# Kernel tuning notes

Measured on AMD Instinct MI355X. Metric: run time of the kernel, lower is better.

Reference implementation:

```python
import jax, jax.numpy as jnp
import numpy as np

WS = 8          # window_size
HEADS = 8
HEAD_DIM = 32
DIM = 256
INNER = HEADS * HEAD_DIM  # 256
STRIDE = 2 * WS - 1       # 15


def _rel_idx_1d():
    # coords of the WS*WS pixels in a window
    coords = np.array([[x, y] for x in range(WS) for y in range(WS)], dtype=np.int32)
    rel = coords[None, :, :] - coords[:, None, :] + (WS - 1)   # [WS^2, WS^2, 2] in [0, 2WS-2]
    idx = rel[:, :, 0] * STRIDE + rel[:, :, 1]
    return jnp.asarray(np.clip(idx, 0, None).reshape(-1), dtype=jnp.int32)

_REL_IDX = _rel_idx_1d()  # [WS^2 * WS^2]


def setup_inputs() -> dict:
    key = jax.random.key(0)
    ks = jax.random.split(key, 5)
    b, l, H, W = 2, 4, 128, 128
    x = jax.random.normal(ks[0], (b, l, H, W, DIM), dtype=jnp.float32)
    W_qkv = jax.random.normal(ks[1], (DIM, 3 * INNER), dtype=jnp.float32) * (DIM ** -0.5)
    W_out = jax.random.normal(ks[2], (INNER, DIM), dtype=jnp.float32) * (INNER ** -0.5)
    b_out = jax.random.normal(ks[3], (DIM,), dtype=jnp.float32) * 0.02
    pos_emb = jax.random.normal(ks[4], (STRIDE, STRIDE), dtype=jnp.float32)
    return {"x": x, "W_qkv": W_qkv, "W_out": W_out, "b_out": b_out, "pos_emb": pos_emb}


def _to_windows(t, b, l, nh, nw):
    # [b,l,H,W,INNER] -> [b,l,heads,nh*nw,WS*WS,head_dim]
    t = t.reshape(b, l, nh, WS, nw, WS, HEADS, HEAD_DIM)
    t = t.transpose(0, 1, 6, 2, 4, 3, 5, 7)  # b l h nh nw ws ws d
    return t.reshape(b, l, HEADS, nh * nw, WS * WS, HEAD_DIM)


def reference(x, W_qkv, W_out, b_out, pos_emb):
    b, l, H, W, _ = x.shape
    nh, nw = H // WS, W // WS
    scale = HEAD_DIM ** -0.5

    qkv = x @ W_qkv                               # [b,l,H,W,3*INNER]
    q, k, v = jnp.split(qkv, 3, axis=-1)
    q = _to_windows(q, b, l, nh, nw)
    k = _to_windows(k, b, l, nh, nw)
    v = _to_windows(v, b, l, nh, nw)

    # per-window attention scores: [b,l,heads,windows,WS^2,WS^2]
    dots = jnp.einsum('blhwid,blhwjd->blhwij', q, k) * scale
    bias = pos_emb.reshape(-1)[_REL_IDX].reshape(WS * WS, WS * WS)
    dots = dots + bias

    attn = jax.nn.softmax(dots, axis=-1)
    out = jnp.einsum('blhwij,blhwjd->blhwid', attn, v)  # [b,l,heads,windows,WS^2,hd]

    # back to [b,l,H,W,INNER]
    out = out.reshape(b, l, HEADS, nh, nw, WS, WS, HEAD_DIM)
    out = out.transpose(0, 1, 3, 5, 4, 6, 2, 7)  # b l nh ws nw ws h d
    out = out.reshape(b, l, nh * WS, nw * WS, INNER)

    return out @ W_out + b_out  # dropout is identity at eval
```

## Files before the change

### kernel.cpp

```cpp
#include <hip/hip_runtime.h>
#include <hip/hip_bf16.h>

typedef short bf16x8 __attribute__((ext_vector_type(8)));
typedef float f32x4  __attribute__((ext_vector_type(4)));
typedef unsigned short u16;
typedef unsigned int u32;

#define MFMA16(a, b, c) __builtin_amdgcn_mfma_f32_16x16x32_bf16((a), (b), (c), 0, 0, 0)

static __device__ __forceinline__ u16 f2b(float f) {
  __hip_bfloat16 h = __float2bfloat16(f);
  return __builtin_bit_cast(u16, h);
}
static __device__ __forceinline__ float b2f(u16 v) {
  unsigned int u = ((unsigned int)v) << 16;
  return __builtin_bit_cast(float, u);
}
static __device__ __forceinline__ u32 pk2(float a, float b) {
  return (u32)f2b(a) | ((u32)f2b(b) << 16);
}

union FragU { uint4 u; bf16x8 v; };

static __device__ __forceinline__ bf16x8 shufx(uint2 lo, uint2 hi,
                                               int sA4, int sB4, bool uh) {
  u32 l0 = (u32)__builtin_amdgcn_ds_bpermute(sA4, (int)lo.x);
  u32 l1 = (u32)__builtin_amdgcn_ds_bpermute(sA4, (int)lo.y);
  u32 h0 = (u32)__builtin_amdgcn_ds_bpermute(sA4, (int)hi.x);
  u32 h1 = (u32)__builtin_amdgcn_ds_bpermute(sA4, (int)hi.y);
  u32 l2 = (u32)__builtin_amdgcn_ds_bpermute(sB4, (int)lo.x);
  u32 l3 = (u32)__builtin_amdgcn_ds_bpermute(sB4, (int)lo.y);
  u32 h2 = (u32)__builtin_amdgcn_ds_bpermute(sB4, (int)hi.x);
  u32 h3 = (u32)__builtin_amdgcn_ds_bpermute(sB4, (int)hi.y);
  FragU f;
  f.u.x = uh ? h0 : l0;  f.u.y = uh ? h1 : l1;
  f.u.z = uh ? h2 : l2;  f.u.w = uh ? h3 : l3;
  return f.v;
}

__global__ void prep(const float* __restrict__ wqkv, const float* __restrict__ wout,
                     const float* __restrict__ pos, u16* __restrict__ wqkT,
                     u16* __restrict__ wvB, u16* __restrict__ woutB,
                     u16* __restrict__ biasQ) {
  const int b = blockIdx.x, t = threadIdx.x;
  const float s = 0.17677669529663689f;
  if (b < 128) {
    int e0 = b * 1024 + t * 4;
#pragma unroll
    for (int i = 0; i < 4; ++i) {
      int e = e0 + i, o = e >> 8, ii = e & 255;
      float v = wqkv[(size_t)ii * 768 + o];
      wqkT[e] = f2b(o < 256 ? v * s : v);
    }
  } else if (b < 192) {
    int e0 = (b - 128) * 1024 + t * 4;
#pragma unroll
    for (int i = 0; i < 4; ++i) {
      int e = e0 + i, frag = e >> 9, w = e & 511, lane = w >> 3, ee = w & 7;
      int k8 = frag >> 4, np = frag & 15;
      int k = k8 * 32 + ((lane >> 4) << 3) + ee;
      int col = 512 + np * 16 + (lane & 15);
      wvB[e] = f2b(wqkv[(size_t)k * 768 + col]);
    }
  } else if (b < 256) {
    int e0 = (b - 192) * 1024 + t * 4;
#pragma unroll
    for (int i = 0; i < 4; ++i) {
      int e = e0 + i, frag = e >> 9, w = e & 511, lane = w >> 3, ee = w & 7;
      int k8 = frag >> 4, np = frag & 15;
      int k = k8 * 32 + ((lane >> 4) << 3) + ee;
      int col = np * 16 + (lane & 15);
      woutB[e] = f2b(wout[(size_t)k * 256 + col]);
    }
  } else {
    int e0 = (b - 256) * 1024 + t * 4;
#pragma unroll
    for (int i = 0; i < 4; ++i) {
      int e = e0 + i, iq = e >> 6, jk = e & 63;
      int ix = iq >> 3, iy = iq & 7, jx = jk >> 3, jy = jk & 7;
      biasQ[e] = f2b(pos[(jx - ix + 7) * 15 + (jy - iy + 7)]);
    }
  }
}

__global__ __launch_bounds__(512, 4)
void winattn(const float* __restrict__ x,
             const u16* __restrict__ wqkT,
             const u16* __restrict__ wvB,
             const u16* __restrict__ woutB,
             const float* __restrict__ b_out,
             const u16* __restrict__ biasQ,
             float* __restrict__ out) {
  __shared__ u16 Xs[64][264];
  __shared__ u16 VTs[256][72];
  __shared__ u16 Bs[64][68];

  const int tid  = threadIdx.x;
  const int lane = tid & 63;
  const int h    = tid >> 6;
  const int c    = lane & 15;
  const int g    = lane >> 4;

  const int win = blockIdx.x;
  const int img = win >> 8;
  const int wid = win & 255;
  const int py0 = (wid >> 4) << 3;
  const int px0 = (wid & 15) << 3;
  const size_t imgbase = (size_t)img * (128 * 128);

  const f32x4 fz = {0.f, 0.f, 0.f, 0.f};

#pragma unroll
  for (int it = 0; it < 8; ++it) {
    int ch = tid + it * 512;
    int row = ch >> 6, c4 = (ch & 63) << 2;
    int py = py0 + (row >> 3), px = px0 + (row & 7);
    const float4 v = *reinterpret_cast<const float4*>(
        x + ((size_t)(imgbase + py * 128 + px)) * 256 + c4);
    ushort4 pk{f2b(v.x), f2b(v.y), f2b(v.z), f2b(v.w)};
    *reinterpret_cast<ushort4*>(&Xs[row][c4]) = pk;
  }
  {
    int row = tid >> 3, c0 = (tid & 7) * 8;
    *reinterpret_cast<ushort4*>(&Bs[row][c0]) =
        *reinterpret_cast<const ushort4*>(biasQ + row * 64 + c0);
    *reinterpret_cast<ushort4*>(&Bs[row][c0 + 4]) =
        *reinterpret_cast<const ushort4*>(biasQ + row * 64 + c0 + 4);
  }
  __syncthreads();

  const int sA4 = (c + 16 * ((2 * g) & 3)) * 4;
  const int sB4 = (c + 16 * ((2 * g + 1) & 3)) * 4;
  const bool uh = g >= 2;

  const int hq = h * 32, hk = 256 + h * 32;

  bf16x8 qf[4];
  {
    f32x4 aq[2][4];
#pragma unroll
    for (int mt = 0; mt < 2; ++mt)
#pragma unroll
      for (int nt = 0; nt < 4; ++nt) aq[mt][nt] = fz;
#pragma unroll 2
    for (int k8 = 0; k8 < 8; ++k8) {
      bf16x8 xb[4];
#pragma unroll
      for (int nt = 0; nt < 4; ++nt)
        xb[nt] = *reinterpret_cast<const bf16x8*>(&Xs[nt * 16 + c][k8 * 32 + g * 8]);
      bf16x8 wq[2];
#pragma unroll
      for (int mt = 0; mt < 2; ++mt)
        wq[mt] = *reinterpret_cast<const bf16x8*>(
            wqkT + (size_t)(hq + mt * 16 + c) * 256 + k8 * 32 + g * 8);
#pragma unroll
      for (int mt = 0; mt < 2; ++mt)
#pragma unroll
        for (int nt = 0; nt < 4; ++nt)
          aq[mt][nt] = MFMA16(wq[mt], xb[nt], aq[mt][nt]);
    }
#pragma unroll
    for (int t4 = 0; t4 < 4; ++t4) {
      uint2 lo{pk2(aq[0][t4][0], aq[0][t4][1]), pk2(aq[0][t4][2], aq[0][t4][3])};
      uint2 hi{pk2(aq[1][t4][0], aq[1][t4][1]), pk2(aq[1][t4][2], aq[1][t4][3])};
      qf[t4] = shufx(lo, hi, sA4, sB4, uh);
    }
  }

  bf16x8 kf[4];
  {
    f32x4 ak[2][4];
#pragma unroll
    for (int mt = 0; mt < 2; ++mt)
#pragma unroll
      for (int nt = 0; nt < 4; ++nt) ak[mt][nt] = fz;
#pragma unroll 2
    for (int k8 = 0; k8 < 8; ++k8) {
      bf16x8 xb[4];
#pragma unroll
      for (int nt = 0; nt < 4; ++nt)
        xb[nt] = *reinterpret_cast<const bf16x8*>(&Xs[nt * 16 + c][k8 * 32 + g * 8]);
      bf16x8 wk[2];
#pragma unroll
      for (int mt = 0; mt < 2; ++mt)
        wk[mt] = *reinterpret_cast<const bf16x8*>(
            wqkT + (size_t)(hk + mt * 16 + c) * 256 + k8 * 32 + g * 8);
#pragma unroll
      for (int mt = 0; mt < 2; ++mt)
#pragma unroll
        for (int nt = 0; nt < 4; ++nt)
          ak[mt][nt] = MFMA16(wk[mt], xb[nt], ak[mt][nt]);
    }
#pragma unroll
    for (int t4 = 0; t4 < 4; ++t4) {
      uint2 lo{pk2(ak[0][t4][0], ak[0][t4][1]), pk2(ak[0][t4][2], ak[0][t4][3])};
      uint2 hi{pk2(ak[1][t4][0], ak[1][t4][1]), pk2(ak[1][t4][2], ak[1][t4][3])};
      kf[t4] = shufx(lo, hi, sA4, sB4, uh);
    }
  }

  {
    f32x4 av[4][2];
#pragma unroll
    for (int mt = 0; mt < 4; ++mt)
#pragma unroll
      for (int j = 0; j < 2; ++j) av[mt][j] = fz;
#pragma unroll 1
    for (int k8 = 0; k8 < 8; ++k8) {
      bf16x8 xb[4];
#pragma unroll
      for (int mt = 0; mt < 4; ++mt)
        xb[mt] = *reinterpret_cast<const bf16x8*>(&Xs[mt * 16 + c][k8 * 32 + g * 8]);
      bf16x8 bv[2];
#pragma unroll
      for (int j = 0; j < 2; ++j)
        bv[j] = *reinterpret_cast<const bf16x8*>(
            wvB + (size_t)((k8 * 16 + 2 * h + j) * 64 + lane) * 8);
#pragma unroll
      for (int mt = 0; mt < 4; ++mt)
#pragma unroll
        for (int j = 0; j < 2; ++j)
          av[mt][j] = MFMA16(xb[mt], bv[j], av[mt][j]);
    }
#pragma unroll
    for (int j = 0; j < 2; ++j)
#pragma unroll
      for (int mt = 0; mt < 4; ++mt) {
        ushort4 pk{f2b(av[mt][j][0]), f2b(av[mt][j][1]),
                   f2b(av[mt][j][2]), f2b(av[mt][j][3])};
        *reinterpret_cast<ushort4*>(&VTs[(2 * h + j) * 16 + c][mt * 16 + 4 * g]) = pk;
      }
  }

  bf16x8 vf[2][2];
#pragma unroll
  for (int kk = 0; kk < 2; ++kk)
#pragma unroll
    for (int dt = 0; dt < 2; ++dt)
      vf[kk][dt] = *reinterpret_cast<const bf16x8*>(
          &VTs[h * 32 + dt * 16 + c][kk * 32 + g * 8]);

  __builtin_amdgcn_s_setprio(1);
  ushort4 ao[8];
#pragma unroll
  for (int tqt = 0; tqt < 4; ++tqt) {
    f32x4 stq[4];
#pragma unroll
    for (int tkt = 0; tkt < 4; ++tkt) {
      const ushort4 bb = *reinterpret_cast<const ushort4*>(
          &Bs[tqt * 16 + c][tkt * 16 + 4 * g]);
      const f32x4 bf = {b2f(bb.x), b2f(bb.y), b2f(bb.z), b2f(bb.w)};
      stq[tkt] = MFMA16(kf[tkt], qf[tqt], bf);
    }
    float m0 = fmaxf(fmaxf(stq[0][0], stq[0][1]), fmaxf(stq[0][2], stq[0][3]));
    float m1 = fmaxf(fmaxf(stq[1][0], stq[1][1]), fmaxf(stq[1][2], stq[1][3]));
    float m2 = fmaxf(fmaxf(stq[2][0], stq[2][1]), fmaxf(stq[2][2], stq[2][3]));
    float m3 = fmaxf(fmaxf(stq[3][0], stq[3][1]), fmaxf(stq[3][2], stq[3][3]));
    float mx = fmaxf(fmaxf(m0, m1), fmaxf(m2, m3));
    mx = fmaxf(mx, __shfl_xor(mx, 16));
    mx = fmaxf(mx, __shfl_xor(mx, 32));
#pragma unroll
    for (int tkt = 0; tkt < 4; ++tkt)
#pragma unroll
      for (int r = 0; r < 4; ++r)
        stq[tkt][r] = __expf(stq[tkt][r] - mx);
    float s0 = (stq[0][0] + stq[0][1]) + (stq[0][2] + stq[0][3]);
    float s1 = (stq[1][0] + stq[1][1]) + (stq[1][2] + stq[1][3]);
    float s2 = (stq[2][0] + stq[2][1]) + (stq[2][2] + stq[2][3]);
    float s3 = (stq[3][0] + stq[3][1]) + (stq[3][2] + stq[3][3]);
    float sum = (s0 + s1) + (s2 + s3);
    sum += __shfl_xor(sum, 16);
    sum += __shfl_xor(sum, 32);
    const float rs = 1.0f / sum;

    f32x4 o0 = fz, o1 = fz;
#pragma unroll
    for (int kk = 0; kk < 2; ++kk) {
      uint2 lo{pk2(stq[2 * kk][0], stq[2 * kk][1]),
               pk2(stq[2 * kk][2], stq[2 * kk][3])};
      uint2 hi{pk2(stq[2 * kk + 1][0], stq[2 * kk + 1][1]),
               pk2(stq[2 * kk + 1][2], stq[2 * kk + 1][3])};
      bf16x8 pf = shufx(lo, hi, sA4, sB4, uh);
      o0 = MFMA16(vf[kk][0], pf, o0);
      o1 = MFMA16(vf[kk][1], pf, o1);
    }
    ao[tqt]     = ushort4{f2b(o0[0] * rs), f2b(o0[1] * rs),
                          f2b(o0[2] * rs), f2b(o0[3] * rs)};
    ao[4 + tqt] = ushort4{f2b(o1[0] * rs), f2b(o1[1] * rs),
                          f2b(o1[2] * rs), f2b(o1[3] * rs)};
  }
  __builtin_amdgcn_s_setprio(0);

  __syncthreads();
#pragma unroll
  for (int dt = 0; dt < 2; ++dt)
#pragma unroll
    for (int tqt = 0; tqt < 4; ++tqt)
      *reinterpret_cast<ushort4*>(&Xs[c + 16 * tqt][h * 32 + 16 * dt + 4 * g]) =
          ao[dt * 4 + tqt];
  __syncthreads();

  f32x4 yc[4][2];
#pragma unroll
  for (int mt = 0; mt < 4; ++mt)
#pragma unroll
    for (int jj = 0; jj < 2; ++jj) yc[mt][jj] = fz;
#pragma unroll 2
  for (int k8 = 0; k8 < 8; ++k8) {
    bf16x8 af[4];
#pragma unroll
    for (int mt = 0; mt < 4; ++mt)
      af[mt] = *reinterpret_cast<const bf16x8*>(&Xs[mt * 16 + c][k8 * 32 + g * 8]);
    bf16x8 bw[2];
#pragma unroll
    for (int jj = 0; jj < 2; ++jj) {
      int nt = h * 2 + jj;
      bw[jj] = *reinterpret_cast<const bf16x8*>(
          woutB + (size_t)((k8 * 16 + nt) * 64 + lane) * 8);
    }
#pragma unroll
    for (int mt = 0; mt < 4; ++mt)
#pragma unroll
      for (int jj = 0; jj < 2; ++jj)
        yc[mt][jj] = MFMA16(af[mt], bw[jj], yc[mt][jj]);
  }
#pragma unroll
  for (int jj = 0; jj < 2; ++jj) {
    const int nt = h * 2 + jj;
    const float bo = b_out[nt * 16 + c];
#pragma unroll
    for (int mt = 0; mt < 4; ++mt)
#pragma unroll
      for (int r = 0; r < 4; ++r) {
        int row = mt * 16 + g * 4 + r;
        int py = py0 + (row >> 3), px = px0 + (row & 7);
        out[((size_t)(imgbase + py * 128 + px)) * 256 + nt * 16 + c] =
            yc[mt][jj][r] + bo;
      }
  }
}

extern "C" void kernel_launch(void* const* d_in, const int* in_sizes, int n_in,
                              void* d_out, int out_size, void* d_ws, size_t ws_size,
                              hipStream_t stream) {
  const float* x    = (const float*)d_in[0];
  const float* wqkv = (const float*)d_in[1];
  const float* wout = (const float*)d_in[2];
  const float* bout = (const float*)d_in[3];
  const float* pos  = (const float*)d_in[4];
  float* out = (float*)d_out;

  u16* wqkT  = (u16*)d_ws;
  u16* wvB   = wqkT + 512 * 256;
  u16* woutB = wvB + 65536;
  u16* biasQ = woutB + 65536;

  prep<<<260, 256, 0, stream>>>(wqkv, wout, pos, wqkT, wvB, woutB, biasQ);
  winattn<<<2048, 512, 0, stream>>>(x, wqkT, wvB, woutB, bout, biasQ, out);
}
```

Before: 138.9 us.

## Drop VTs shared buffer, build V fragments in registers, raise occupancy

V projection output is now shuffled straight into MFMA B-fragments in registers instead of going through a transposed shared-memory buffer. This removes about 36KB of LDS per block. Q and K projections are computed one half at a time to cut live accumulators, and attention outputs are written directly into Xs after a barrier. Launch bounds request 6 blocks per CU. The combined aim is higher occupancy, at the risk of register spills or a worse MFMA schedule from the smaller per-iteration tiles.

```diff
diff --git a/kernel.cpp b/kernel.cpp
--- a/kernel.cpp
+++ b/kernel.cpp
@@ -83,7 +83,7 @@
   }
 }
 
-__global__ __launch_bounds__(512, 4)
+__global__ __launch_bounds__(512, 6)
 void winattn(const float* __restrict__ x,
              const u16* __restrict__ wqkT,
              const u16* __restrict__ wvB,
@@ -92,7 +92,6 @@
              const u16* __restrict__ biasQ,
              float* __restrict__ out) {
   __shared__ u16 Xs[64][264];
-  __shared__ u16 VTs[256][72];
   __shared__ u16 Bs[64][68];
 
   const int tid  = threadIdx.x;
@@ -135,70 +134,7 @@
 
   const int hq = h * 32, hk = 256 + h * 32;
 
-  bf16x8 qf[4];
-  {
-    f32x4 aq[2][4];
-#pragma unroll
-    for (int mt = 0; mt < 2; ++mt)
-#pragma unroll
-      for (int nt = 0; nt < 4; ++nt) aq[mt][nt] = fz;
-#pragma unroll 2
-    for (int k8 = 0; k8 < 8; ++k8) {
-      bf16x8 xb[4];
-#pragma unroll
-      for (int nt = 0; nt < 4; ++nt)
-        xb[nt] = *reinterpret_cast<const bf16x8*>(&Xs[nt * 16 + c][k8 * 32 + g * 8]);
-      bf16x8 wq[2];
-#pragma unroll
-      for (int mt = 0; mt < 2; ++mt)
-        wq[mt] = *reinterpret_cast<const bf16x8*>(
-            wqkT + (size_t)(hq + mt * 16 + c) * 256 + k8 * 32 + g * 8);
-#pragma unroll
-      for (int mt = 0; mt < 2; ++mt)
-#pragma unroll
-        for (int nt = 0; nt < 4; ++nt)
-          aq[mt][nt] = MFMA16(wq[mt], xb[nt], aq[mt][nt]);
-    }
-#pragma unroll
-    for (int t4 = 0; t4 < 4; ++t4) {
-      uint2 lo{pk2(aq[0][t4][0], aq[0][t4][1]), pk2(aq[0][t4][2], aq[0][t4][3])};
-      uint2 hi{pk2(aq[1][t4][0], aq[1][t4][1]), pk2(aq[1][t4][2], aq[1][t4][3])};
-      qf[t4] = shufx(lo, hi, sA4, sB4, uh);
-    }
-  }
-
-  bf16x8 kf[4];
-  {
-    f32x4 ak[2][4];
-#pragma unroll
-    for (int mt = 0; mt < 2; ++mt)
-#pragma unroll
-      for (int nt = 0; nt < 4; ++nt) ak[mt][nt] = fz;
-#pragma unroll 2
-    for (int k8 = 0; k8 < 8; ++k8) {
-      bf16x8 xb[4];
-#pragma unroll
-      for (int nt = 0; nt < 4; ++nt)
-        xb[nt] = *reinterpret_cast<const bf16x8*>(&Xs[nt * 16 + c][k8 * 32 + g * 8]);
-      bf16x8 wk[2];
-#pragma unroll
-      for (int mt = 0; mt < 2; ++mt)
-        wk[mt] = *reinterpret_cast<const bf16x8*>(
-            wqkT + (size_t)(hk + mt * 16 + c) * 256 + k8 * 32 + g * 8);
-#pragma unroll
-      for (int mt = 0; mt < 2; ++mt)
-#pragma unroll
-        for (int nt = 0; nt < 4; ++nt)
-          ak[mt][nt] = MFMA16(wk[mt], xb[nt], ak[mt][nt]);
-    }
-#pragma unroll
-    for (int t4 = 0; t4 < 4; ++t4) {
-      uint2 lo{pk2(ak[0][t4][0], ak[0][t4][1]), pk2(ak[0][t4][2], ak[0][t4][3])};
-      uint2 hi{pk2(ak[1][t4][0], ak[1][t4][1]), pk2(ak[1][t4][2], ak[1][t4][3])};
-      kf[t4] = shufx(lo, hi, sA4, sB4, uh);
-    }
-  }
-
+  bf16x8 vf[2][2];
   {
     f32x4 av[4][2];
 #pragma unroll
@@ -225,23 +161,80 @@
 #pragma unroll
     for (int j = 0; j < 2; ++j)
 #pragma unroll
-      for (int mt = 0; mt < 4; ++mt) {
-        ushort4 pk{f2b(av[mt][j][0]), f2b(av[mt][j][1]),
-                   f2b(av[mt][j][2]), f2b(av[mt][j][3])};
-        *reinterpret_cast<ushort4*>(&VTs[(2 * h + j) * 16 + c][mt * 16 + 4 * g]) = pk;
-      }
-  }
-
-  bf16x8 vf[2][2];
-#pragma unroll
-  for (int kk = 0; kk < 2; ++kk)
-#pragma unroll
-    for (int dt = 0; dt < 2; ++dt)
-      vf[kk][dt] = *reinterpret_cast<const bf16x8*>(
-          &VTs[h * 32 + dt * 16 + c][kk * 32 + g * 8]);
+      for (int kk = 0; kk < 2; ++kk) {
+        uint2 lo{pk2(av[2 * kk][j][0], av[2 * kk][j][1]),
+                 pk2(av[2 * kk][j][2], av[2 * kk][j][3])};
+        uint2 hi{pk2(av[2 * kk + 1][j][0], av[2 * kk + 1][j][1]),
+                 pk2(av[2 * kk + 1][j][2], av[2 * kk + 1][j][3])};
+        vf[kk][j] = shufx(lo, hi, sA4, sB4, uh);
+      }
+  }
+
+  bf16x8 qf[4];
+  {
+    uint2 qlo[4], qhi[4];
+#pragma unroll
+    for (int mt = 0; mt < 2; ++mt) {
+      f32x4 aq[4];
+#pragma unroll
+      for (int nt = 0; nt < 4; ++nt) aq[nt] = fz;
+#pragma unroll 2
+      for (int k8 = 0; k8 < 8; ++k8) {
+        bf16x8 xb[4];
+#pragma unroll
+        for (int nt = 0; nt < 4; ++nt)
+          xb[nt] = *reinterpret_cast<const bf16x8*>(&Xs[nt * 16 + c][k8 * 32 + g * 8]);
+        const bf16x8 wq = *reinterpret_cast<const bf16x8*>(
+            wqkT + (size_t)(hq + mt * 16 + c) * 256 + k8 * 32 + g * 8);
+#pragma unroll
+        for (int nt = 0; nt < 4; ++nt)
+          aq[nt] = MFMA16(wq, xb[nt], aq[nt]);
+      }
+#pragma unroll
+      for (int t4 = 0; t4 < 4; ++t4) {
+        uint2 pk{pk2(aq[t4][0], aq[t4][1]), pk2(aq[t4][2], aq[t4][3])};
+        if (mt == 0) qlo[t4] = pk; else qhi[t4] = pk;
+      }
+    }
+#pragma unroll
+    for (int t4 = 0; t4 < 4; ++t4)
+      qf[t4] = shufx(qlo[t4], qhi[t4], sA4, sB4, uh);
+  }
+
+  bf16x8 kf[4];
+  {
+    uint2 klo[4], khi[4];
+#pragma unroll
+    for (int mt = 0; mt < 2; ++mt) {
+      f32x4 ak[4];
+#pragma unroll
+      for (int nt = 0; nt < 4; ++nt) ak[nt] = fz;
+#pragma unroll 2
+      for (int k8 = 0; k8 < 8; ++k8) {
+        bf16x8 xb[4];
+#pragma unroll
+        for (int nt = 0; nt < 4; ++nt)
+          xb[nt] = *reinterpret_cast<const bf16x8*>(&Xs[nt * 16 + c][k8 * 32 + g * 8]);
+        const bf16x8 wk = *reinterpret_cast<const bf16x8*>(
+            wqkT + (size_t)(hk + mt * 16 + c) * 256 + k8 * 32 + g * 8);
+#pragma unroll
+        for (int nt = 0; nt < 4; ++nt)
+          ak[nt] = MFMA16(wk, xb[nt], ak[nt]);
+      }
+#pragma unroll
+      for (int t4 = 0; t4 < 4; ++t4) {
+        uint2 pk{pk2(ak[t4][0], ak[t4][1]), pk2(ak[t4][2], ak[t4][3])};
+        if (mt == 0) klo[t4] = pk; else khi[t4] = pk;
+      }
+    }
+#pragma unroll
+    for (int t4 = 0; t4 < 4; ++t4)
+      kf[t4] = shufx(klo[t4], khi[t4], sA4, sB4, uh);
+  }
+
+  __syncthreads();
 
   __builtin_amdgcn_s_setprio(1);
-  ushort4 ao[8];
 #pragma unroll
   for (int tqt = 0; tqt < 4; ++tqt) {
     f32x4 stq[4];
@@ -284,20 +277,13 @@
       o0 = MFMA16(vf[kk][0], pf, o0);
       o1 = MFMA16(vf[kk][1], pf, o1);
     }
-    ao[tqt]     = ushort4{f2b(o0[0] * rs), f2b(o0[1] * rs),
-                          f2b(o0[2] * rs), f2b(o0[3] * rs)};
-    ao[4 + tqt] = ushort4{f2b(o1[0] * rs), f2b(o1[1] * rs),
-                          f2b(o1[2] * rs), f2b(o1[3] * rs)};
+    *reinterpret_cast<ushort4*>(&Xs[c + 16 * tqt][h * 32 + 4 * g]) =
+        ushort4{f2b(o0[0] * rs), f2b(o0[1] * rs), f2b(o0[2] * rs), f2b(o0[3] * rs)};
+    *reinterpret_cast<ushort4*>(&Xs[c + 16 * tqt][h * 32 + 16 + 4 * g]) =
+        ushort4{f2b(o1[0] * rs), f2b(o1[1] * rs), f2b(o1[2] * rs), f2b(o1[3] * rs)};
   }
   __builtin_amdgcn_s_setprio(0);
 
-  __syncthreads();
-#pragma unroll
-  for (int dt = 0; dt < 2; ++dt)
-#pragma unroll
-    for (int tqt = 0; tqt < 4; ++tqt)
-      *reinterpret_cast<ushort4*>(&Xs[c + 16 * tqt][h * 32 + 16 * dt + 4 * g]) =
-          ao[dt * 4 + tqt];
   __syncthreads();
 
   f32x4 yc[4][2];
```

New measurement: 182.6 us. +31.5%, slower.
